# Kernel optimization log

Measured on AMD Instinct MI355X. Metric: run time of the kernel, lower is better.

The kernel has to match this reference:

```python
import jax, jax.numpy as jnp
import numpy as np

N = 100000       # nodes
E = 1600000      # edges (avg degree 16)
D_IN = 128
D_HID = 128      # 2 * out_channels
D_OUT = 64
BN_EPS = 1e-5
LRELU_SLOPE = 0.01
NORM_SCALE = 1.8


def setup_inputs() -> dict:
    key = jax.random.key(0)
    ks = jax.random.split(key, 8)
    x = jax.random.normal(ks[0], (N, D_IN), dtype=jnp.float32)
    edge_src = jax.random.randint(ks[1], (E,), 0, N)
    edge_dst = jax.random.randint(ks[2], (E,), 0, N)
    W1 = jax.random.normal(ks[3], (D_IN, D_HID), dtype=jnp.float32) / np.sqrt(D_IN).astype(np.float32)
    b1 = jnp.zeros((D_HID,), jnp.float32)
    gamma = jnp.ones((D_HID,), jnp.float32)
    beta = jnp.zeros((D_HID,), jnp.float32)
    Wmu = jax.random.normal(ks[4], (D_HID, D_OUT), dtype=jnp.float32) / np.sqrt(D_HID).astype(np.float32)
    bmu = jnp.zeros((D_OUT,), jnp.float32)
    noise = jax.random.normal(ks[5], (N, D_OUT), dtype=jnp.float32)
    return {"x": x, "edge_src": edge_src, "edge_dst": edge_dst, "W1": W1, "b1": b1,
            "gamma": gamma, "beta": beta, "Wmu": Wmu, "bmu": bmu, "noise": noise}


def appnp_k1(x, src, dst):
    """APPNP(K=1, alpha=0) == one symmetric GCN-normalized SpMM with self-loops."""
    ones = jnp.ones((src.shape[0],), x.dtype)
    deg = jax.ops.segment_sum(ones, dst, num_segments=N) + 1.0  # +1 for self-loop
    dinv = jax.lax.rsqrt(deg)
    w = dinv[src] * dinv[dst]                                   # [E] edge weights
    agg = jax.ops.segment_sum(x[src] * w[:, None], dst, num_segments=N)
    return agg + x * (dinv * dinv)[:, None]                     # self-loop term


def reference(x, edge_src, edge_dst, W1, b1, gamma, beta, Wmu, bmu, noise):
    # conv1 + propagate
    h = x @ W1 + b1                         # [N, D_HID]
    h = appnp_k1(h, edge_src, edge_dst)
    # BatchNorm1d (training mode: batch stats, biased variance)
    mean = h.mean(axis=0)
    var = h.var(axis=0)
    h = gamma * (h - mean) * jax.lax.rsqrt(var + BN_EPS) + beta
    # LeakyReLU
    h = jnp.where(h > 0, h, LRELU_SLOPE * h)
    # mu branch (convmu + propagate)
    l = h @ Wmu + bmu                       # [N, D_OUT]; used for both mu and logstd (original reuses convmu)
    mu = appnp_k1(l, edge_src, edge_dst)
    # logstd branch: F.normalize(convmu(h), p=2, dim=1) * 1.8 then propagate
    nrm = jnp.maximum(jnp.linalg.norm(l, axis=1, keepdims=True), 1e-12)
    logstd = appnp_k1(l / nrm * NORM_SCALE, edge_src, edge_dst)
    # reparam (training): mu + eps * exp(logstd)
    zeta = mu + noise * jnp.exp(logstd)
    return (mu, logstd, zeta)
```

## Files before the change

kernel.cpp:

```cpp
#include <hip/hip_runtime.h>
#include <hip/hip_bf16.h>
#include <math.h>

#define D_IN 128
#define D_HID 128
#define D_OUT 64
#define BN_EPS 1e-5f
#define SLOPE 0.01f
#define NSCALE 1.8f

#define BSH 8
#define NB 256
#define T1 4096
#define COLCAP 8192
#define LSTRIDE 192

typedef __attribute__((ext_vector_type(8))) short short8;
typedef __attribute__((ext_vector_type(4))) float f32x4;

__device__ inline void atomAddF(float* p, float v) {
#if defined(__gfx90a__) || defined(__gfx942__) || defined(__gfx950__)
    unsafeAtomicAdd(p, v);
#else
    atomicAdd(p, v);
#endif
}

__device__ inline ushort f2bf(float f) {
    union { float f; uint u; } v; v.f = f;
    uint r = v.u + 0x7fff + ((v.u >> 16) & 1);
    return (ushort)(r >> 16);
}
__device__ inline float bf2f(ushort b) {
    union { uint u; float f; } v; v.u = ((uint)b) << 16;
    return v.f;
}
__device__ inline float bflo(uint u) { return __uint_as_float(u << 16); }
__device__ inline float bfhi(uint u) { return __uint_as_float(u & 0xffff0000u); }

__device__ inline void add4(uint2 v, float a[4]) {
    a[0] += bflo(v.x); a[1] += bfhi(v.x);
    a[2] += bflo(v.y); a[3] += bfhi(v.y);
}
__device__ inline void fma4(uint2 v, float w, float a[4]) {
    a[0] = fmaf(bflo(v.x), w, a[0]);
    a[1] = fmaf(bfhi(v.x), w, a[1]);
    a[2] = fmaf(bflo(v.y), w, a[2]);
    a[3] = fmaf(bfhi(v.y), w, a[3]);
}
__device__ inline void acc8(uint4 v, float sv, float w, float am[8], float al[8]) {
    float e;
    e = bflo(v.x) * w; am[0] += e; al[0] = fmaf(e, sv, al[0]);
    e = bfhi(v.x) * w; am[1] += e; al[1] = fmaf(e, sv, al[1]);
    e = bflo(v.y) * w; am[2] += e; al[2] = fmaf(e, sv, al[2]);
    e = bfhi(v.y) * w; am[3] += e; al[3] = fmaf(e, sv, al[3]);
    e = bflo(v.z) * w; am[4] += e; al[4] = fmaf(e, sv, al[4]);
    e = bfhi(v.z) * w; am[5] += e; al[5] = fmaf(e, sv, al[5]);
    e = bflo(v.w) * w; am[6] += e; al[6] = fmaf(e, sv, al[6]);
    e = bfhi(v.w) * w; am[7] += e; al[7] = fmaf(e, sv, al[7]);
}

__global__ __launch_bounds__(256) void k_bhist(const int* __restrict__ dst,
        int* __restrict__ bcnt, int E, int B) {
    __shared__ int h[512];
    for (int i = threadIdx.x; i < 512; i += 256) h[i] = 0;
    __syncthreads();
    int beg = blockIdx.x * T1;
    int end = min(beg + T1, E);
    for (int e = beg + threadIdx.x; e < end; e += 256)
        atomicAdd(&h[dst[e] >> BSH], 1);
    __syncthreads();
    for (int i = threadIdx.x; i < B; i += 256)
        if (h[i]) atomicAdd(&bcnt[i], h[i]);
}

__global__ __launch_bounds__(512) void k_bscan(const int* __restrict__ bcnt,
        int* __restrict__ bbase, int* __restrict__ tailE, int B) {
    __shared__ int sh[512];
    int t = threadIdx.x;
    int v = (t < B) ? bcnt[t] : 0;
    sh[t] = v;
    __syncthreads();
    for (int o = 1; o < 512; o <<= 1) {
        int u = (t >= o) ? sh[t - o] : 0;
        __syncthreads();
        sh[t] += u;
        __syncthreads();
    }
    int excl = sh[t] - v;
    if (t < B) { bbase[t] = excl; tailE[t] = excl; }
    if (t == B - 1) bbase[B] = excl + v;
}

__global__ __launch_bounds__(256) void k_part(const int* __restrict__ src,
        const int* __restrict__ dst, int* __restrict__ tailE,
        uint* __restrict__ ep, int E, int B) {
    __shared__ int h[512], off[512], gb[512], cur[512];
    __shared__ int ps[256];
    __shared__ int2 ro[T1];
    int tid = threadIdx.x;
    for (int i = tid; i < 512; i += 256) h[i] = 0;
    __syncthreads();
    int beg = blockIdx.x * T1;
    int cnt = min(T1, E - beg);
    int s[16], d[16];
#pragma unroll
    for (int k = 0; k < 16; ++k) {
        int e = beg + tid + k * 256;
        if (e < E) {
            s[k] = src[e]; d[k] = dst[e];
            atomicAdd(&h[d[k] >> BSH], 1);
        } else d[k] = -1;
    }
    __syncthreads();
    int pa = h[2 * tid], pb = h[2 * tid + 1];
    ps[tid] = pa + pb;
    __syncthreads();
    int vv = ps[tid];
    for (int o = 1; o < 256; o <<= 1) {
        int u = (tid >= o) ? ps[tid - o] : 0;
        __syncthreads();
        ps[tid] += u;
        __syncthreads();
    }
    int excl = ps[tid] - vv;
    off[2 * tid] = excl;       off[2 * tid + 1] = excl + pa;
    cur[2 * tid] = excl;       cur[2 * tid + 1] = excl + pa;
    if (2 * tid < B && pa > 0)      gb[2 * tid] = atomicAdd(&tailE[2 * tid], pa);
    if (2 * tid + 1 < B && pb > 0)  gb[2 * tid + 1] = atomicAdd(&tailE[2 * tid + 1], pb);
    __syncthreads();
#pragma unroll
    for (int k = 0; k < 16; ++k) {
        if (d[k] >= 0) {
            int b = d[k] >> BSH;
            int p = atomicAdd(&cur[b], 1);
            ro[p] = make_int2(s[k], d[k]);
        }
    }
    __syncthreads();
    for (int i = tid; i < cnt; i += 256) {
        int2 e = ro[i];
        int b = e.y >> BSH;
        ep[gb[b] + (i - off[b])] = (uint)e.x | ((uint)(e.y & (NB - 1)) << 24);
    }
}

__global__ __launch_bounds__(256) void k_csr(const uint* __restrict__ ep,
        const int* __restrict__ bbase, int* __restrict__ rowptr,
        float* __restrict__ dinv, int* __restrict__ col, int n, int B) {
    int b = blockIdx.x;
    int lo = b << BSH;
    int hi = min(lo + NB, n);
    int nn = hi - lo;
    int ebeg = bbase[b], eend = bbase[b + 1], cnt = eend - ebeg;
    __shared__ int h[NB], pfx[NB], cur[NB];
    __shared__ int colbuf[COLCAP];
    int tid = threadIdx.x;
    if (tid < NB) h[tid] = 0;
    __syncthreads();
    for (int i = tid; i < cnt; i += 256)
        atomicAdd(&h[ep[ebeg + i] >> 24], 1);
    __syncthreads();
    int v = (tid < nn) ? h[tid] : 0;
    pfx[tid] = v;
    __syncthreads();
    for (int o = 1; o < 256; o <<= 1) {
        int u = (tid >= o) ? pfx[tid - o] : 0;
        __syncthreads();
        pfx[tid] += u;
        __syncthreads();
    }
    int excl = pfx[tid] - v;
    if (tid < nn) {
        rowptr[lo + tid] = ebeg + excl;
        dinv[lo + tid] = rsqrtf((float)v + 1.0f);
        cur[tid] = excl;
    }
    if (b == B - 1 && tid == 0) rowptr[n] = eend;
    __syncthreads();
    if (cnt <= COLCAP) {
        for (int i = tid; i < cnt; i += 256) {
            uint e = ep[ebeg + i];
            int p = atomicAdd(&cur[e >> 24], 1);
            colbuf[p] = (int)(e & 0xFFFFFFu);
        }
        __syncthreads();
        for (int i = tid; i < cnt; i += 256) col[ebeg + i] = colbuf[i];
    } else {
        for (int i = tid; i < cnt; i += 256) {
            uint e = ep[ebeg + i];
            int p = atomicAdd(&cur[e >> 24], 1);
            col[ebeg + p] = (int)(e & 0xFFFFFFu);
        }
    }
}

__global__ __launch_bounds__(256) void k_gemm1_mfma(const float* __restrict__ x,
        const float* __restrict__ W1, const float* __restrict__ b1,
        const float* __restrict__ dinv, ushort* __restrict__ h_bf, int n, int nwt) {
    __shared__ ushort wf[4][8][64][8];
    int t = threadIdx.x;
    for (int i = t; i < 16384; i += 256) {
        int k = i >> 7, nn = i & 127;
        int kt = k >> 5, ct = nn >> 4;
        int lane = ((k >> 3) & 3) * 16 + (nn & 15);
        int j = k & 7;
        wf[kt][ct][lane][j] = f2bf(W1[i]);
    }
    __syncthreads();
    size_t n64 = (size_t)n * 64;
    int wid = t >> 6, lane = t & 63;
    int lrow = lane & 15, lkg = lane >> 4;
    float bias[8];
#pragma unroll
    for (int ct = 0; ct < 8; ++ct) bias[ct] = b1[ct * 16 + lrow];
    int stride = gridDim.x * 4;
    for (int wt = blockIdx.x * 4 + wid; wt < nwt; wt += stride) {
        size_t r0 = (size_t)wt * 16;
        int rr = (int)r0 + lrow;
        if (rr >= n) rr = n - 1;
        short8 ah[4], al[4];
#pragma unroll
        for (int kt = 0; kt < 4; ++kt) {
            const float* p = x + (size_t)rr * 128 + kt * 32 + lkg * 8;
            float va[8];
            *(f32x4*)&va[0] = *(const f32x4*)p;
            *(f32x4*)&va[4] = *(const f32x4*)(p + 4);
#pragma unroll
            for (int j = 0; j < 8; ++j) {
                ushort hb = f2bf(va[j]);
                ah[kt][j] = (short)hb;
                al[kt][j] = (short)f2bf(va[j] - bf2f(hb));
            }
        }
        f32x4 acc[8];
#pragma unroll
        for (int ct = 0; ct < 8; ++ct) {
            float bb = bias[ct];
            acc[ct][0] = bb; acc[ct][1] = bb; acc[ct][2] = bb; acc[ct][3] = bb;
        }
#pragma unroll
        for (int kt = 0; kt < 4; ++kt) {
#pragma unroll
            for (int ct = 0; ct < 8; ++ct) {
                short8 wh = *(const short8*)&wf[kt][ct][lane][0];
                acc[ct] = __builtin_amdgcn_mfma_f32_16x16x32_bf16(ah[kt], wh, acc[ct], 0, 0, 0);
                acc[ct] = __builtin_amdgcn_mfma_f32_16x16x32_bf16(al[kt], wh, acc[ct], 0, 0, 0);
            }
        }
#pragma unroll
        for (int j = 0; j < 4; ++j) {
            int row = (int)r0 + lkg * 4 + j;
            if (row < n) {
                float dr = dinv[row];
#pragma unroll
                for (int ct = 0; ct < 8; ++ct)
                    h_bf[(size_t)(ct >> 2) * n64 + (size_t)row * 64 + (ct & 3) * 16 + lrow]
                        = f2bf(acc[ct][j] * dr);
            }
        }
    }
}

__global__ __launch_bounds__(512) void k_spmm1_csr(const int* __restrict__ rowptr,
        const int* __restrict__ col, const uint2* __restrict__ tbl,
        const float* __restrict__ dinv, uint2* __restrict__ aggq,
        float* __restrict__ accum, int n, int half) {
    __shared__ float red[8][16][4];
    int t = threadIdx.x;
    int wid = t >> 6, lane = t & 63;
    int q = lane >> 4, g = lane & 15;
    int gw = blockIdx.x * 8 + wid;
    int nw = gridDim.x * 8;
    float sx[4] = {0.f, 0.f, 0.f, 0.f}, sq[4] = {0.f, 0.f, 0.f, 0.f};
    for (int node = gw; node < n; node += nw) {
        int beg = rowptr[node], end = rowptr[node + 1];
        float a[4] = {0.f, 0.f, 0.f, 0.f};
        if (q == 0) add4(tbl[(size_t)node * 16 + g], a);
        int p = beg;
        for (; p + 16 <= end; p += 16) {
            int c0 = col[p + q], c1 = col[p + 4 + q];
            int c2 = col[p + 8 + q], c3 = col[p + 12 + q];
            uint2 v0 = tbl[(size_t)c0 * 16 + g];
            uint2 v1 = tbl[(size_t)c1 * 16 + g];
            uint2 v2 = tbl[(size_t)c2 * 16 + g];
            uint2 v3 = tbl[(size_t)c3 * 16 + g];
            add4(v0, a); add4(v1, a); add4(v2, a); add4(v3, a);
        }
        if (p + 8 <= end) {
            int c0 = col[p + q], c1 = col[p + 4 + q];
            uint2 v0 = tbl[(size_t)c0 * 16 + g];
            uint2 v1 = tbl[(size_t)c1 * 16 + g];
            add4(v0, a); add4(v1, a);
            p += 8;
        }
        if (p < end) {
            int i0 = p + q, i1 = p + 4 + q;
            int c0 = col[i0 < end ? i0 : end - 1];
            int c1 = col[i1 < end ? i1 : end - 1];
            float w0 = (i0 < end) ? 1.f : 0.f;
            float w1 = (i1 < end) ? 1.f : 0.f;
            fma4(tbl[(size_t)c0 * 16 + g], w0, a);
            fma4(tbl[(size_t)c1 * 16 + g], w1, a);
        }
#pragma unroll
        for (int j = 0; j < 4; ++j) {
            a[j] += __shfl_xor(a[j], 16, 64);
            a[j] += __shfl_xor(a[j], 32, 64);
        }
        if (q == 0) {
            float di = dinv[node];
#pragma unroll
            for (int j = 0; j < 4; ++j) a[j] *= di;
            uint2 pk;
            pk.x = ((uint)f2bf(a[1]) << 16) | (uint)f2bf(a[0]);
            pk.y = ((uint)f2bf(a[3]) << 16) | (uint)f2bf(a[2]);
            aggq[(size_t)node * 32 + half * 16 + g] = pk;
#pragma unroll
            for (int j = 0; j < 4; ++j) {
                sx[j] += a[j];
                sq[j] = fmaf(a[j], a[j], sq[j]);
            }
        }
    }
    if (q == 0) {
#pragma unroll
        for (int j = 0; j < 4; ++j) red[wid][g][j] = sx[j];
    }
    __syncthreads();
    if (t < 64) {
        float v = 0.f;
        for (int w = 0; w < 8; ++w) v += red[w][t >> 2][t & 3];
        atomAddF(&accum[half * 64 + t], v);
    }
    __syncthreads();
    if (q == 0) {
#pragma unroll
        for (int j = 0; j < 4; ++j) red[wid][g][j] = sq[j];
    }
    __syncthreads();
    if (t < 64) {
        float v = 0.f;
        for (int w = 0; w < 8; ++w) v += red[w][t >> 2][t & 3];
        atomAddF(&accum[128 + half * 64 + t], v);
    }
}

__global__ __launch_bounds__(256) void k_gemm2_mfma(const ushort* __restrict__ agg_bf,
        const float* __restrict__ Wmu, const float* __restrict__ bmu,
        const float* __restrict__ accum, const float* __restrict__ gamma,
        const float* __restrict__ beta, const float* __restrict__ dinv,
        char* __restrict__ l_ext, float inv_n, int n, int nwt) {
    __shared__ ushort wf[4][4][64][8];
    __shared__ float scs[D_HID], shs[D_HID];
    int t = threadIdx.x;
    for (int i = t; i < 8192; i += 256) {
        int k = i >> 6, nn = i & 63;
        int kt = k >> 5, ct = nn >> 4;
        int lane = ((k >> 3) & 3) * 16 + (nn & 15);
        int j = k & 7;
        wf[kt][ct][lane][j] = f2bf(Wmu[i]);
    }
    for (int i = t; i < D_HID; i += 256) {
        float mean = accum[i] * inv_n;
        float var = accum[D_HID + i] * inv_n - mean * mean;
        float sc = gamma[i] * rsqrtf(var + BN_EPS);
        scs[i] = sc;
        shs[i] = beta[i] - mean * sc;
    }
    __syncthreads();
    int wid = t >> 6, lane = t & 63;
    int lrow = lane & 15, lkg = lane >> 4;
    float bias[4];
#pragma unroll
    for (int ct = 0; ct < 4; ++ct) bias[ct] = bmu[ct * 16 + lrow];
    int stride = gridDim.x * 4;
    for (int wt = blockIdx.x * 4 + wid; wt < nwt; wt += stride) {
        size_t r0 = (size_t)wt * 16;
        int rr = (int)r0 + lrow;
        if (rr >= n) rr = n - 1;
        short8 ah[4], al[4];
#pragma unroll
        for (int kt = 0; kt < 4; ++kt) {
            const ushort* p = agg_bf + (size_t)rr * 128 + kt * 32 + lkg * 8;
            short8 raw = *(const short8*)p;
#pragma unroll
            for (int j = 0; j < 8; ++j) {
                int k = kt * 32 + lkg * 8 + j;
                float v = bf2f((ushort)raw[j]) * scs[k] + shs[k];
                v = v > 0.f ? v : SLOPE * v;
                ushort hb = f2bf(v);
                ah[kt][j] = (short)hb;
                al[kt][j] = (short)f2bf(v - bf2f(hb));
            }
        }
        f32x4 acc[4];
#pragma unroll
        for (int ct = 0; ct < 4; ++ct) {
            float bb = bias[ct];
            acc[ct][0] = bb; acc[ct][1] = bb; acc[ct][2] = bb; acc[ct][3] = bb;
        }
#pragma unroll
        for (int kt = 0; kt < 4; ++kt) {
#pragma unroll
            for (int ct = 0; ct < 4; ++ct) {
                short8 wh = *(const short8*)&wf[kt][ct][lane][0];
                acc[ct] = __builtin_amdgcn_mfma_f32_16x16x32_bf16(ah[kt], wh, acc[ct], 0, 0, 0);
                acc[ct] = __builtin_amdgcn_mfma_f32_16x16x32_bf16(al[kt], wh, acc[ct], 0, 0, 0);
            }
        }
#pragma unroll
        for (int j = 0; j < 4; ++j) {
            float ss = acc[0][j] * acc[0][j];
#pragma unroll
            for (int ct = 1; ct < 4; ++ct) ss = fmaf(acc[ct][j], acc[ct][j], ss);
            ss += __shfl_xor(ss, 1, 64);
            ss += __shfl_xor(ss, 2, 64);
            ss += __shfl_xor(ss, 4, 64);
            ss += __shfl_xor(ss, 8, 64);
            float srow = NSCALE / fmaxf(sqrtf(ss), 1e-12f);
            int row = (int)r0 + lkg * 4 + j;
            if (row < n) {
                float dr = dinv[row];
                char* base = l_ext + (size_t)row * LSTRIDE;
#pragma unroll
                for (int ct = 0; ct < 4; ++ct)
                    *(ushort*)(base + (ct * 16 + lrow) * 2) = f2bf(acc[ct][j] * dr);
                if (lrow == 0) *(float*)(base + 128) = srow;
            }
        }
    }
}

__global__ __launch_bounds__(512) void k_spmm2_csr(const int* __restrict__ rowptr,
        const int* __restrict__ col, const char* __restrict__ lb,
        const float* __restrict__ dinv, const float* __restrict__ noise,
        float* __restrict__ mu, float* __restrict__ lsd, float* __restrict__ zeta,
        int n) {
    int node = blockIdx.x * 8 + ((int)threadIdx.x >> 6);
    if (node >= n) return;
    int lane = threadIdx.x & 63;
    int oct = lane >> 3, g = lane & 7;
    int beg = rowptr[node], end = rowptr[node + 1];
    float am[8], al[8];
#pragma unroll
    for (int j = 0; j < 8; ++j) { am[j] = 0.f; al[j] = 0.f; }
    if (oct == 0) {
        const char* rb = lb + (size_t)node * LSTRIDE;
        uint4 v = *(const uint4*)(rb + g * 16);
        float sv = *(const float*)(rb + 128);
        acc8(v, sv, 1.f, am, al);
    }
    int p = beg;
    for (; p + 16 <= end; p += 16) {
        int c0 = col[p + oct], c1 = col[p + 8 + oct];
        const char* r0 = lb + (size_t)c0 * LSTRIDE;
        const char* r1 = lb + (size_t)c1 * LSTRIDE;
        uint4 v0 = *(const uint4*)(r0 + g * 16);
        float s0 = *(const float*)(r0 + 128);
        uint4 v1 = *(const uint4*)(r1 + g * 16);
        float s1 = *(const float*)(r1 + 128);
        acc8(v0, s0, 1.f, am, al);
        acc8(v1, s1, 1.f, am, al);
    }
    if (p + 8 <= end) {
        int c0 = col[p + oct];
        const char* r0 = lb + (size_t)c0 * LSTRIDE;
        uint4 v0 = *(const uint4*)(r0 + g * 16);
        float s0 = *(const float*)(r0 + 128);
        acc8(v0, s0, 1.f, am, al);
        p += 8;
    }
    if (p < end) {
        int i0 = p + oct;
        int c0 = col[i0 < end ? i0 : end - 1];
        float w0 = (i0 < end) ? 1.f : 0.f;
        const char* r0 = lb + (size_t)c0 * LSTRIDE;
        uint4 v0 = *(const uint4*)(r0 + g * 16);
        float s0 = *(const float*)(r0 + 128);
        acc8(v0, s0, w0, am, al);
    }
#pragma unroll
    for (int j = 0; j < 8; ++j) {
        am[j] += __shfl_xor(am[j], 8, 64);
        am[j] += __shfl_xor(am[j], 16, 64);
        am[j] += __shfl_xor(am[j], 32, 64);
        al[j] += __shfl_xor(al[j], 8, 64);
        al[j] += __shfl_xor(al[j], 16, 64);
        al[j] += __shfl_xor(al[j], 32, 64);
    }
    if (lane < 8) {
        float di = dinv[node];
        size_t idx = (size_t)node * 64 + lane * 8;
        f32x4 m0, m1, l0, l1, z0, z1;
#pragma unroll
        for (int j = 0; j < 4; ++j) {
            m0[j] = am[j] * di;     m1[j] = am[j + 4] * di;
            l0[j] = al[j] * di;     l1[j] = al[j + 4] * di;
        }
        f32x4 n0 = *(const f32x4*)(noise + idx);
        f32x4 n1 = *(const f32x4*)(noise + idx + 4);
#pragma unroll
        for (int j = 0; j < 4; ++j) {
            z0[j] = m0[j] + n0[j] * expf(l0[j]);
            z1[j] = m1[j] + n1[j] * expf(l1[j]);
        }
        *(f32x4*)(mu + idx) = m0;   *(f32x4*)(mu + idx + 4) = m1;
        *(f32x4*)(lsd + idx) = l0;  *(f32x4*)(lsd + idx + 4) = l1;
        *(f32x4*)(zeta + idx) = z0; *(f32x4*)(zeta + idx + 4) = z1;
    }
}

extern "C" void kernel_launch(void* const* d_in, const int* in_sizes, int n_in,
                              void* d_out, int out_size, void* d_ws, size_t ws_size,
                              hipStream_t stream) {
    const float* x     = (const float*)d_in[0];
    const int*   esrc  = (const int*)d_in[1];
    const int*   edst  = (const int*)d_in[2];
    const float* W1    = (const float*)d_in[3];
    const float* b1    = (const float*)d_in[4];
    const float* gamma = (const float*)d_in[5];
    const float* beta  = (const float*)d_in[6];
    const float* Wmu   = (const float*)d_in[7];
    const float* bmu   = (const float*)d_in[8];
    const float* noise = (const float*)d_in[9];
    int N = in_sizes[0] / D_IN;
    int E = in_sizes[1];
    int B = (N + NB - 1) >> BSH;
    int nwt = (N + 15) / 16;
    int ntile = (E + T1 - 1) / T1;

    float* out  = (float*)d_out;
    float* mu   = out;
    float* lsd  = out + (size_t)N * D_OUT;
    float* zeta = out + 2 * (size_t)N * D_OUT;

    char* ws = (char*)d_ws;
    size_t off = 0;
    auto alloc = [&](size_t bytes) {
        void* p = ws + off;
        off += (bytes + 255) & ~(size_t)255;
        return p;
    };
    float* accum  = (float*)alloc(1024);
    int* bcnt     = (int*)alloc((size_t)B * 4);
    size_t zbytes = off;
    int* bbase    = (int*)alloc(((size_t)B + 1) * 4);
    int* tailE    = (int*)alloc((size_t)B * 4);
    int* rowptr   = (int*)alloc(((size_t)N + 1) * 4);
    float* dinv   = (float*)alloc((size_t)N * 4);
    uint* ep      = (uint*)alloc((size_t)E * 4);
    int* col      = (int*)alloc((size_t)E * 4);
    ushort* h_bf  = (ushort*)alloc((size_t)N * D_HID * 2);
    uint2* aggq   = (uint2*)alloc((size_t)N * D_HID * 2);
    char* l_ext   = (char*)alloc((size_t)N * LSTRIDE);

    hipMemsetAsync(d_ws, 0, zbytes, stream);

    size_t n64 = (size_t)N * 64;
    const uint2* tbl0 = (const uint2*)h_bf;
    const uint2* tbl1 = (const uint2*)(h_bf + n64);

    k_bhist<<<ntile, 256, 0, stream>>>(edst, bcnt, E, B);
    k_bscan<<<1, 512, 0, stream>>>(bcnt, bbase, tailE, B);
    k_part<<<ntile, 256, 0, stream>>>(esrc, edst, tailE, ep, E, B);
    k_csr<<<B, 256, 0, stream>>>(ep, bbase, rowptr, dinv, col, N, B);
    k_gemm1_mfma<<<512, 256, 0, stream>>>(x, W1, b1, dinv, h_bf, N, nwt);
    k_spmm1_csr<<<2048, 512, 0, stream>>>(rowptr, col, tbl0, dinv, aggq, accum, N, 0);
    k_spmm1_csr<<<2048, 512, 0, stream>>>(rowptr, col, tbl1, dinv, aggq, accum, N, 1);
    k_gemm2_mfma<<<512, 256, 0, stream>>>((const ushort*)aggq, Wmu, bmu, accum,
                                          gamma, beta, dinv, l_ext, 1.0f / (float)N, N, nwt);
    k_spmm2_csr<<<(N + 7) / 8, 512, 0, stream>>>(rowptr, col, l_ext, dinv, noise, mu, lsd, zeta, N);
}
```

Baseline: 311.6 us.

## Map one 16-lane group per node in both SpMM kernels, dropping cross-lane reductions

Both SpMM kernels now assign a 16-thread group to each destination node, with every lane walking all of that node's edges serially, instead of splitting edges across the 4 or 8 lane groups of a wavefront and combining them with shuffles. This removes the shuffle reductions and leaves no lanes idle during the epilogue, and it lets each kernel handle four times as many nodes per block. In exchange, each lane issues more dependent gather loads per node, and the memory access per node is narrower (uint2 rather than uint4 in spmm2). The BatchNorm statistics reduction now uses shared-memory atomics instead of a per-wave array.

New measurement: 355.4 us. 1.14x slower.

```diff
diff --git a/kernel.cpp b/kernel.cpp
--- a/kernel.cpp
+++ b/kernel.cpp
@@ -48,16 +48,12 @@
     a[2] = fmaf(bflo(v.y), w, a[2]);
     a[3] = fmaf(bfhi(v.y), w, a[3]);
 }
-__device__ inline void acc8(uint4 v, float sv, float w, float am[8], float al[8]) {
+__device__ inline void dacc4(uint2 v, float sv, float w, float am[4], float al[4]) {
     float e;
     e = bflo(v.x) * w; am[0] += e; al[0] = fmaf(e, sv, al[0]);
     e = bfhi(v.x) * w; am[1] += e; al[1] = fmaf(e, sv, al[1]);
     e = bflo(v.y) * w; am[2] += e; al[2] = fmaf(e, sv, al[2]);
     e = bfhi(v.y) * w; am[3] += e; al[3] = fmaf(e, sv, al[3]);
-    e = bflo(v.z) * w; am[4] += e; al[4] = fmaf(e, sv, al[4]);
-    e = bfhi(v.z) * w; am[5] += e; al[5] = fmaf(e, sv, al[5]);
-    e = bflo(v.w) * w; am[6] += e; al[6] = fmaf(e, sv, al[6]);
-    e = bfhi(v.w) * w; am[7] += e; al[7] = fmaf(e, sv, al[7]);
 }
 
 __global__ __launch_bounds__(256) void k_bhist(const int* __restrict__ dst,
@@ -266,83 +262,65 @@
         const int* __restrict__ col, const uint2* __restrict__ tbl,
         const float* __restrict__ dinv, uint2* __restrict__ aggq,
         float* __restrict__ accum, int n, int half) {
-    __shared__ float red[8][16][4];
+    __shared__ float redx[64], redq[64];
     int t = threadIdx.x;
-    int wid = t >> 6, lane = t & 63;
-    int q = lane >> 4, g = lane & 15;
-    int gw = blockIdx.x * 8 + wid;
-    int nw = gridDim.x * 8;
+    if (t < 64) { redx[t] = 0.f; redq[t] = 0.f; }
+    __syncthreads();
+    int grp = t >> 4, lid = t & 15;
+    int nstride = gridDim.x * 32;
     float sx[4] = {0.f, 0.f, 0.f, 0.f}, sq[4] = {0.f, 0.f, 0.f, 0.f};
-    for (int node = gw; node < n; node += nw) {
+    for (int node = blockIdx.x * 32 + grp; node < n; node += nstride) {
         int beg = rowptr[node], end = rowptr[node + 1];
         float a[4] = {0.f, 0.f, 0.f, 0.f};
-        if (q == 0) add4(tbl[(size_t)node * 16 + g], a);
+        add4(tbl[(size_t)node * 16 + lid], a);
         int p = beg;
-        for (; p + 16 <= end; p += 16) {
-            int c0 = col[p + q], c1 = col[p + 4 + q];
-            int c2 = col[p + 8 + q], c3 = col[p + 12 + q];
-            uint2 v0 = tbl[(size_t)c0 * 16 + g];
-            uint2 v1 = tbl[(size_t)c1 * 16 + g];
-            uint2 v2 = tbl[(size_t)c2 * 16 + g];
-            uint2 v3 = tbl[(size_t)c3 * 16 + g];
+        for (; p + 8 <= end; p += 8) {
+            int c0 = col[p],     c1 = col[p + 1], c2 = col[p + 2], c3 = col[p + 3];
+            int c4 = col[p + 4], c5 = col[p + 5], c6 = col[p + 6], c7 = col[p + 7];
+            uint2 v0 = tbl[(size_t)c0 * 16 + lid];
+            uint2 v1 = tbl[(size_t)c1 * 16 + lid];
+            uint2 v2 = tbl[(size_t)c2 * 16 + lid];
+            uint2 v3 = tbl[(size_t)c3 * 16 + lid];
+            uint2 v4 = tbl[(size_t)c4 * 16 + lid];
+            uint2 v5 = tbl[(size_t)c5 * 16 + lid];
+            uint2 v6 = tbl[(size_t)c6 * 16 + lid];
+            uint2 v7 = tbl[(size_t)c7 * 16 + lid];
             add4(v0, a); add4(v1, a); add4(v2, a); add4(v3, a);
-        }
-        if (p + 8 <= end) {
-            int c0 = col[p + q], c1 = col[p + 4 + q];
-            uint2 v0 = tbl[(size_t)c0 * 16 + g];
-            uint2 v1 = tbl[(size_t)c1 * 16 + g];
-            add4(v0, a); add4(v1, a);
-            p += 8;
-        }
-        if (p < end) {
-            int i0 = p + q, i1 = p + 4 + q;
-            int c0 = col[i0 < end ? i0 : end - 1];
-            int c1 = col[i1 < end ? i1 : end - 1];
-            float w0 = (i0 < end) ? 1.f : 0.f;
-            float w1 = (i1 < end) ? 1.f : 0.f;
-            fma4(tbl[(size_t)c0 * 16 + g], w0, a);
-            fma4(tbl[(size_t)c1 * 16 + g], w1, a);
-        }
+            add4(v4, a); add4(v5, a); add4(v6, a); add4(v7, a);
+        }
+        if (p + 4 <= end) {
+            int c0 = col[p], c1 = col[p + 1], c2 = col[p + 2], c3 = col[p + 3];
+            uint2 v0 = tbl[(size_t)c0 * 16 + lid];
+            uint2 v1 = tbl[(size_t)c1 * 16 + lid];
+            uint2 v2 = tbl[(size_t)c2 * 16 + lid];
+            uint2 v3 = tbl[(size_t)c3 * 16 + lid];
+            add4(v0, a); add4(v1, a); add4(v2, a); add4(v3, a);
+            p += 4;
+        }
+        for (; p < end; ++p)
+            add4(tbl[(size_t)col[p] * 16 + lid], a);
+        float di = dinv[node];
+#pragma unroll
+        for (int j = 0; j < 4; ++j) a[j] *= di;
+        uint2 pk;
+        pk.x = ((uint)f2bf(a[1]) << 16) | (uint)f2bf(a[0]);
+        pk.y = ((uint)f2bf(a[3]) << 16) | (uint)f2bf(a[2]);
+        aggq[(size_t)node * 32 + half * 16 + lid] = pk;
 #pragma unroll
         for (int j = 0; j < 4; ++j) {
-            a[j] += __shfl_xor(a[j], 16, 64);
-            a[j] += __shfl_xor(a[j], 32, 64);
-        }
-        if (q == 0) {
-            float di = dinv[node];
-#pragma unroll
-            for (int j = 0; j < 4; ++j) a[j] *= di;
-            uint2 pk;
-            pk.x = ((uint)f2bf(a[1]) << 16) | (uint)f2bf(a[0]);
-            pk.y = ((uint)f2bf(a[3]) << 16) | (uint)f2bf(a[2]);
-            aggq[(size_t)node * 32 + half * 16 + g] = pk;
-#pragma unroll
-            for (int j = 0; j < 4; ++j) {
-                sx[j] += a[j];
-                sq[j] = fmaf(a[j], a[j], sq[j]);
-            }
-        }
-    }
-    if (q == 0) {
-#pragma unroll
-        for (int j = 0; j < 4; ++j) red[wid][g][j] = sx[j];
+            sx[j] += a[j];
+            sq[j] = fmaf(a[j], a[j], sq[j]);
+        }
+    }
+#pragma unroll
+    for (int j = 0; j < 4; ++j) {
+        atomicAdd(&redx[lid * 4 + j], sx[j]);
+        atomicAdd(&redq[lid * 4 + j], sq[j]);
     }
     __syncthreads();
     if (t < 64) {
-        float v = 0.f;
-        for (int w = 0; w < 8; ++w) v += red[w][t >> 2][t & 3];
-        atomAddF(&accum[half * 64 + t], v);
-    }
-    __syncthreads();
-    if (q == 0) {
-#pragma unroll
-        for (int j = 0; j < 4; ++j) red[wid][g][j] = sq[j];
-    }
-    __syncthreads();
-    if (t < 64) {
-        float v = 0.f;
-        for (int w = 0; w < 8; ++w) v += red[w][t >> 2][t & 3];
-        atomAddF(&accum[128 + half * 64 + t], v);
+        atomAddF(&accum[half * 64 + t], redx[t]);
+        atomAddF(&accum[128 + half * 64 + t], redq[t]);
     }
 }
 
@@ -437,78 +415,74 @@
         const float* __restrict__ dinv, const float* __restrict__ noise,
         float* __restrict__ mu, float* __restrict__ lsd, float* __restrict__ zeta,
         int n) {
-    int node = blockIdx.x * 8 + ((int)threadIdx.x >> 6);
+    int t = threadIdx.x;
+    int grp = t >> 4, lid = t & 15;
+    int node = blockIdx.x * 32 + grp;
     if (node >= n) return;
-    int lane = threadIdx.x & 63;
-    int oct = lane >> 3, g = lane & 7;
     int beg = rowptr[node], end = rowptr[node + 1];
-    float am[8], al[8];
-#pragma unroll
-    for (int j = 0; j < 8; ++j) { am[j] = 0.f; al[j] = 0.f; }
-    if (oct == 0) {
+    float am[4] = {0.f, 0.f, 0.f, 0.f}, al[4] = {0.f, 0.f, 0.f, 0.f};
+    {
         const char* rb = lb + (size_t)node * LSTRIDE;
-        uint4 v = *(const uint4*)(rb + g * 16);
+        uint2 v = *(const uint2*)(rb + lid * 8);
         float sv = *(const float*)(rb + 128);
-        acc8(v, sv, 1.f, am, al);
+        dacc4(v, sv, 1.f, am, al);
     }
     int p = beg;
-    for (; p + 16 <= end; p += 16) {
-        int c0 = col[p + oct], c1 = col[p + 8 + oct];
+    for (; p + 8 <= end; p += 8) {
+        int c0 = col[p],     c1 = col[p + 1], c2 = col[p + 2], c3 = col[p + 3];
+        int c4 = col[p + 4], c5 = col[p + 5], c6 = col[p + 6], c7 = col[p + 7];
         const char* r0 = lb + (size_t)c0 * LSTRIDE;
         const char* r1 = lb + (size_t)c1 * LSTRIDE;
-        uint4 v0 = *(const uint4*)(r0 + g * 16);
+        const char* r2 = lb + (size_t)c2 * LSTRIDE;
+        const char* r3 = lb + (size_t)c3 * LSTRIDE;
+        const char* r4 = lb + (size_t)c4 * LSTRIDE;
+        const char* r5 = lb + (size_t)c5 * LSTRIDE;
+        const char* r6 = lb + (size_t)c6 * LSTRIDE;
+        const char* r7 = lb + (size_t)c7 * LSTRIDE;
+        uint2 v0 = *(const uint2*)(r0 + lid * 8); float s0 = *(const float*)(r0 + 128);
+        uint2 v1 = *(const uint2*)(r1 + lid * 8); float s1 = *(const float*)(r1 + 128);
+        uint2 v2 = *(const uint2*)(r2 + lid * 8); float s2 = *(const float*)(r2 + 128);
+        uint2 v3 = *(const uint2*)(r3 + lid * 8); float s3 = *(const float*)(r3 + 128);
+        uint2 v4 = *(const uint2*)(r4 + lid * 8); float s4 = *(const float*)(r4 + 128);
+        uint2 v5 = *(const uint2*)(r5 + lid * 8); float s5 = *(const float*)(r5 + 128);
+        uint2 v6 = *(const uint2*)(r6 + lid * 8); float s6 = *(const float*)(r6 + 128);
+        uint2 v7 = *(const uint2*)(r7 + lid * 8); float s7 = *(const float*)(r7 + 128);
+        dacc4(v0, s0, 1.f, am, al); dacc4(v1, s1, 1.f, am, al);
+        dacc4(v2, s2, 1.f, am, al); dacc4(v3, s3, 1.f, am, al);
+        dacc4(v4, s4, 1.f, am, al); dacc4(v5, s5, 1.f, am, al);
+        dacc4(v6, s6, 1.f, am, al); dacc4(v7, s7, 1.f, am, al);
+    }
+    if (p + 4 <= end) {
+        int c0 = col[p], c1 = col[p + 1], c2 = col[p + 2], c3 = col[p + 3];
+        const char* r0 = lb + (size_t)c0 * LSTRIDE;
+        const char* r1 = lb + (size_t)c1 * LSTRIDE;
+        const char* r2 = lb + (size_t)c2 * LSTRIDE;
+        const char* r3 = lb + (size_t)c3 * LSTRIDE;
+        uint2 v0 = *(const uint2*)(r0 + lid * 8); float s0 = *(const float*)(r0 + 128);
+        uint2 v1 = *(const uint2*)(r1 + lid * 8); float s1 = *(const float*)(r1 + 128);
+        uint2 v2 = *(const uint2*)(r2 + lid * 8); float s2 = *(const float*)(r2 + 128);
+        uint2 v3 = *(const uint2*)(r3 + lid * 8); float s3 = *(const float*)(r3 + 128);
+        dacc4(v0, s0, 1.f, am, al); dacc4(v1, s1, 1.f, am, al);
+        dacc4(v2, s2, 1.f, am, al); dacc4(v3, s3, 1.f, am, al);
+        p += 4;
+    }
+    for (; p < end; ++p) {
+        const char* r0 = lb + (size_t)col[p] * LSTRIDE;
+        uint2 v0 = *(const uint2*)(r0 + lid * 8);
         float s0 = *(const float*)(r0 + 128);
-        uint4 v1 = *(const uint4*)(r1 + g * 16);
-        float s1 = *(const float*)(r1 + 128);
-        acc8(v0, s0, 1.f, am, al);
-        acc8(v1, s1, 1.f, am, al);
-    }
-    if (p + 8 <= end) {
-        int c0 = col[p + oct];
-        const char* r0 = lb + (size_t)c0 * LSTRIDE;
-        uint4 v0 = *(const uint4*)(r0 + g * 16);
-        float s0 = *(const float*)(r0 + 128);
-        acc8(v0, s0, 1.f, am, al);
-        p += 8;
-    }
-    if (p < end) {
-        int i0 = p + oct;
-        int c0 = col[i0 < end ? i0 : end - 1];
-        float w0 = (i0 < end) ? 1.f : 0.f;
-        const char* r0 = lb + (size_t)c0 * LSTRIDE;
-        uint4 v0 = *(const uint4*)(r0 + g * 16);
-        float s0 = *(const float*)(r0 + 128);
-        acc8(v0, s0, w0, am, al);
-    }
-#pragma unroll
-    for (int j = 0; j < 8; ++j) {
-        am[j] += __shfl_xor(am[j], 8, 64);
-        am[j] += __shfl_xor(am[j], 16, 64);
-        am[j] += __shfl_xor(am[j], 32, 64);
-        al[j] += __shfl_xor(al[j], 8, 64);
-        al[j] += __shfl_xor(al[j], 16, 64);
-        al[j] += __shfl_xor(al[j], 32, 64);
-    }
-    if (lane < 8) {
-        float di = dinv[node];
-        size_t idx = (size_t)node * 64 + lane * 8;
-        f32x4 m0, m1, l0, l1, z0, z1;
-#pragma unroll
-        for (int j = 0; j < 4; ++j) {
-            m0[j] = am[j] * di;     m1[j] = am[j + 4] * di;
-            l0[j] = al[j] * di;     l1[j] = al[j + 4] * di;
-        }
-        f32x4 n0 = *(const f32x4*)(noise + idx);
-        f32x4 n1 = *(const f32x4*)(noise + idx + 4);
-#pragma unroll
-        for (int j = 0; j < 4; ++j) {
-            z0[j] = m0[j] + n0[j] * expf(l0[j]);
-            z1[j] = m1[j] + n1[j] * expf(l1[j]);
-        }
-        *(f32x4*)(mu + idx) = m0;   *(f32x4*)(mu + idx + 4) = m1;
-        *(f32x4*)(lsd + idx) = l0;  *(f32x4*)(lsd + idx + 4) = l1;
-        *(f32x4*)(zeta + idx) = z0; *(f32x4*)(zeta + idx + 4) = z1;
-    }
+        dacc4(v0, s0, 1.f, am, al);
+    }
+    float di = dinv[node];
+    size_t idx = (size_t)node * 64 + lid * 4;
+    f32x4 m, l, z;
+#pragma unroll
+    for (int j = 0; j < 4; ++j) { m[j] = am[j] * di; l[j] = al[j] * di; }
+    f32x4 nz = *(const f32x4*)(noise + idx);
+#pragma unroll
+    for (int j = 0; j < 4; ++j) z[j] = m[j] + nz[j] * expf(l[j]);
+    *(f32x4*)(mu + idx) = m;
+    *(f32x4*)(lsd + idx) = l;
+    *(f32x4*)(zeta + idx) = z;
 }
 
 extern "C" void kernel_launch(void* const* d_in, const int* in_sizes, int n_in,
@@ -570,5 +544,5 @@
     k_spmm1_csr<<<2048, 512, 0, stream>>>(rowptr, col, tbl1, dinv, aggq, accum, N, 1);
     k_gemm2_mfma<<<512, 256, 0, stream>>>((const ushort*)aggq, Wmu, bmu, accum,
                                           gamma, beta, dinv, l_ext, 1.0f / (float)N, N, nwt);
-    k_spmm2_csr<<<(N + 7) / 8, 512, 0, stream>>>(rowptr, col, l_ext, dinv, noise, mu, lsd, zeta, N);
-}
+    k_spmm2_csr<<<(N + 31) / 32, 512, 0, stream>>>(rowptr, col, l_ext, dinv, noise, mu, lsd, zeta, N);
+}
```

## Switch SpMM gathers to fp16 packed math and merge halved SpMM1 passes

Applied to the files above, without the earlier changes.

Intermediate feature tables are now stored as fp16 instead of bf16. The gathers accumulate with packed half2 add and fma instead of unpacking to fp32, and the cross-lane reductions in SpMM2 run on half2 as well. The two half-width SpMM1 launches are merged into one pass over the full 128-wide row using 16-byte loads, which halves the CSR/index traffic and the launch count. The cost is reduced accumulation precision: fp16 sums over about 17 neighbours carry a risk of overflow or tolerance failures.

Measured after the change: 271.5 us. 1.15x faster.

```diff
diff --git a/kernel.cpp b/kernel.cpp
--- a/kernel.cpp
+++ b/kernel.cpp
@@ -1,5 +1,6 @@
 #include <hip/hip_runtime.h>
 #include <hip/hip_bf16.h>
+#include <hip/hip_fp16.h>
 #include <math.h>
 
 #define D_IN 128
@@ -35,29 +36,29 @@
     union { uint u; float f; } v; v.u = ((uint)b) << 16;
     return v.f;
 }
-__device__ inline float bflo(uint u) { return __uint_as_float(u << 16); }
-__device__ inline float bfhi(uint u) { return __uint_as_float(u & 0xffff0000u); }
-
-__device__ inline void add4(uint2 v, float a[4]) {
-    a[0] += bflo(v.x); a[1] += bfhi(v.x);
-    a[2] += bflo(v.y); a[3] += bfhi(v.y);
-}
-__device__ inline void fma4(uint2 v, float w, float a[4]) {
-    a[0] = fmaf(bflo(v.x), w, a[0]);
-    a[1] = fmaf(bfhi(v.x), w, a[1]);
-    a[2] = fmaf(bflo(v.y), w, a[2]);
-    a[3] = fmaf(bfhi(v.y), w, a[3]);
-}
-__device__ inline void acc8(uint4 v, float sv, float w, float am[8], float al[8]) {
-    float e;
-    e = bflo(v.x) * w; am[0] += e; al[0] = fmaf(e, sv, al[0]);
-    e = bfhi(v.x) * w; am[1] += e; al[1] = fmaf(e, sv, al[1]);
-    e = bflo(v.y) * w; am[2] += e; al[2] = fmaf(e, sv, al[2]);
-    e = bfhi(v.y) * w; am[3] += e; al[3] = fmaf(e, sv, al[3]);
-    e = bflo(v.z) * w; am[4] += e; al[4] = fmaf(e, sv, al[4]);
-    e = bfhi(v.z) * w; am[5] += e; al[5] = fmaf(e, sv, al[5]);
-    e = bflo(v.w) * w; am[6] += e; al[6] = fmaf(e, sv, al[6]);
-    e = bfhi(v.w) * w; am[7] += e; al[7] = fmaf(e, sv, al[7]);
+__device__ inline ushort f2h(float f) {
+    __half h = __float2half_rn(f);
+    return *reinterpret_cast<ushort*>(&h);
+}
+__device__ inline __half2 u2h2(uint u) { return *reinterpret_cast<__half2*>(&u); }
+__device__ inline __half2 shfl_xor_h2(__half2 v, int m) {
+    int iv = *reinterpret_cast<int*>(&v);
+    int r = __shfl_xor(iv, m, 64);
+    return *reinterpret_cast<__half2*>(&r);
+}
+
+__device__ inline void phadd8(uint4 v, __half2 a[4]) {
+    a[0] = __hadd2(a[0], u2h2(v.x));
+    a[1] = __hadd2(a[1], u2h2(v.y));
+    a[2] = __hadd2(a[2], u2h2(v.z));
+    a[3] = __hadd2(a[3], u2h2(v.w));
+}
+__device__ inline void pdacc8(uint4 v, __half2 s2, __half2 am[4], __half2 al[4]) {
+    __half2 h0 = u2h2(v.x), h1 = u2h2(v.y), h2 = u2h2(v.z), h3 = u2h2(v.w);
+    am[0] = __hadd2(am[0], h0); al[0] = __hfma2(h0, s2, al[0]);
+    am[1] = __hadd2(am[1], h1); al[1] = __hfma2(h1, s2, al[1]);
+    am[2] = __hadd2(am[2], h2); al[2] = __hfma2(h2, s2, al[2]);
+    am[3] = __hadd2(am[3], h3); al[3] = __hfma2(h3, s2, al[3]);
 }
 
 __global__ __launch_bounds__(256) void k_bhist(const int* __restrict__ dst,
@@ -197,7 +198,7 @@
 
 __global__ __launch_bounds__(256) void k_gemm1_mfma(const float* __restrict__ x,
         const float* __restrict__ W1, const float* __restrict__ b1,
-        const float* __restrict__ dinv, ushort* __restrict__ h_bf, int n, int nwt) {
+        const float* __restrict__ dinv, ushort* __restrict__ h16, int n, int nwt) {
     __shared__ ushort wf[4][8][64][8];
     int t = threadIdx.x;
     for (int i = t; i < 16384; i += 256) {
@@ -208,7 +209,6 @@
         wf[kt][ct][lane][j] = f2bf(W1[i]);
     }
     __syncthreads();
-    size_t n64 = (size_t)n * 64;
     int wid = t >> 6, lane = t & 63;
     int lrow = lane & 15, lkg = lane >> 4;
     float bias[8];
@@ -255,69 +255,79 @@
                 float dr = dinv[row];
 #pragma unroll
                 for (int ct = 0; ct < 8; ++ct)
-                    h_bf[(size_t)(ct >> 2) * n64 + (size_t)row * 64 + (ct & 3) * 16 + lrow]
-                        = f2bf(acc[ct][j] * dr);
+                    h16[(size_t)row * 128 + ct * 16 + lrow] = f2h(acc[ct][j] * dr);
             }
         }
     }
 }
 
 __global__ __launch_bounds__(512) void k_spmm1_csr(const int* __restrict__ rowptr,
-        const int* __restrict__ col, const uint2* __restrict__ tbl,
-        const float* __restrict__ dinv, uint2* __restrict__ aggq,
-        float* __restrict__ accum, int n, int half) {
-    __shared__ float red[8][16][4];
+        const int* __restrict__ col, const uint4* __restrict__ tbl,
+        const float* __restrict__ dinv, uint4* __restrict__ agg4,
+        float* __restrict__ accum, int n) {
+    __shared__ float red[8][16][8];
     int t = threadIdx.x;
     int wid = t >> 6, lane = t & 63;
     int q = lane >> 4, g = lane & 15;
     int gw = blockIdx.x * 8 + wid;
     int nw = gridDim.x * 8;
-    float sx[4] = {0.f, 0.f, 0.f, 0.f}, sq[4] = {0.f, 0.f, 0.f, 0.f};
+    float sx[8], sq[8];
+#pragma unroll
+    for (int j = 0; j < 8; ++j) { sx[j] = 0.f; sq[j] = 0.f; }
+    __half2 hz = __float2half2_rn(0.f);
     for (int node = gw; node < n; node += nw) {
         int beg = rowptr[node], end = rowptr[node + 1];
-        float a[4] = {0.f, 0.f, 0.f, 0.f};
-        if (q == 0) add4(tbl[(size_t)node * 16 + g], a);
+        __half2 a2[4] = {hz, hz, hz, hz};
+        if (q == 0) phadd8(tbl[(size_t)node * 16 + g], a2);
         int p = beg;
         for (; p + 16 <= end; p += 16) {
             int c0 = col[p + q], c1 = col[p + 4 + q];
             int c2 = col[p + 8 + q], c3 = col[p + 12 + q];
-            uint2 v0 = tbl[(size_t)c0 * 16 + g];
-            uint2 v1 = tbl[(size_t)c1 * 16 + g];
-            uint2 v2 = tbl[(size_t)c2 * 16 + g];
-            uint2 v3 = tbl[(size_t)c3 * 16 + g];
-            add4(v0, a); add4(v1, a); add4(v2, a); add4(v3, a);
+            uint4 v0 = tbl[(size_t)c0 * 16 + g];
+            uint4 v1 = tbl[(size_t)c1 * 16 + g];
+            uint4 v2 = tbl[(size_t)c2 * 16 + g];
+            uint4 v3 = tbl[(size_t)c3 * 16 + g];
+            phadd8(v0, a2); phadd8(v1, a2); phadd8(v2, a2); phadd8(v3, a2);
         }
         if (p + 8 <= end) {
             int c0 = col[p + q], c1 = col[p + 4 + q];
-            uint2 v0 = tbl[(size_t)c0 * 16 + g];
-            uint2 v1 = tbl[(size_t)c1 * 16 + g];
-            add4(v0, a); add4(v1, a);
+            uint4 v0 = tbl[(size_t)c0 * 16 + g];
+            uint4 v1 = tbl[(size_t)c1 * 16 + g];
+            phadd8(v0, a2); phadd8(v1, a2);
             p += 8;
         }
         if (p < end) {
             int i0 = p + q, i1 = p + 4 + q;
             int c0 = col[i0 < end ? i0 : end - 1];
             int c1 = col[i1 < end ? i1 : end - 1];
-            float w0 = (i0 < end) ? 1.f : 0.f;
-            float w1 = (i1 < end) ? 1.f : 0.f;
-            fma4(tbl[(size_t)c0 * 16 + g], w0, a);
-            fma4(tbl[(size_t)c1 * 16 + g], w1, a);
-        }
+            uint4 v0 = tbl[(size_t)c0 * 16 + g];
+            uint4 v1 = tbl[(size_t)c1 * 16 + g];
+            if (i0 < end) phadd8(v0, a2);
+            if (i1 < end) phadd8(v1, a2);
+        }
+        float a[8];
 #pragma unroll
         for (int j = 0; j < 4; ++j) {
+            float2 f = __half22float2(a2[j]);
+            a[2 * j] = f.x; a[2 * j + 1] = f.y;
+        }
+#pragma unroll
+        for (int j = 0; j < 8; ++j) {
             a[j] += __shfl_xor(a[j], 16, 64);
             a[j] += __shfl_xor(a[j], 32, 64);
         }
         if (q == 0) {
             float di = dinv[node];
 #pragma unroll
-            for (int j = 0; j < 4; ++j) a[j] *= di;
-            uint2 pk;
+            for (int j = 0; j < 8; ++j) a[j] *= di;
+            uint4 pk;
             pk.x = ((uint)f2bf(a[1]) << 16) | (uint)f2bf(a[0]);
             pk.y = ((uint)f2bf(a[3]) << 16) | (uint)f2bf(a[2]);
-            aggq[(size_t)node * 32 + half * 16 + g] = pk;
-#pragma unroll
-            for (int j = 0; j < 4; ++j) {
+            pk.z = ((uint)f2bf(a[5]) << 16) | (uint)f2bf(a[4]);
+            pk.w = ((uint)f2bf(a[7]) << 16) | (uint)f2bf(a[6]);
+            agg4[(size_t)node * 16 + g] = pk;
+#pragma unroll
+            for (int j = 0; j < 8; ++j) {
                 sx[j] += a[j];
                 sq[j] = fmaf(a[j], a[j], sq[j]);
             }
@@ -325,24 +335,24 @@
     }
     if (q == 0) {
 #pragma unroll
-        for (int j = 0; j < 4; ++j) red[wid][g][j] = sx[j];
-    }
-    __syncthreads();
-    if (t < 64) {
+        for (int j = 0; j < 8; ++j) red[wid][g][j] = sx[j];
+    }
+    __syncthreads();
+    if (t < 128) {
         float v = 0.f;
-        for (int w = 0; w < 8; ++w) v += red[w][t >> 2][t & 3];
-        atomAddF(&accum[half * 64 + t], v);
+        for (int w = 0; w < 8; ++w) v += red[w][t >> 3][t & 7];
+        atomAddF(&accum[t], v);
     }
     __syncthreads();
     if (q == 0) {
 #pragma unroll
-        for (int j = 0; j < 4; ++j) red[wid][g][j] = sq[j];
-    }
-    __syncthreads();
-    if (t < 64) {
+        for (int j = 0; j < 8; ++j) red[wid][g][j] = sq[j];
+    }
+    __syncthreads();
+    if (t < 128) {
         float v = 0.f;
-        for (int w = 0; w < 8; ++w) v += red[w][t >> 2][t & 3];
-        atomAddF(&accum[128 + half * 64 + t], v);
+        for (int w = 0; w < 8; ++w) v += red[w][t >> 3][t & 7];
+        atomAddF(&accum[128 + t], v);
     }
 }
 
@@ -425,8 +435,8 @@
                 char* base = l_ext + (size_t)row * LSTRIDE;
 #pragma unroll
                 for (int ct = 0; ct < 4; ++ct)
-                    *(ushort*)(base + (ct * 16 + lrow) * 2) = f2bf(acc[ct][j] * dr);
-                if (lrow == 0) *(float*)(base + 128) = srow;
+                    *(ushort*)(base + (ct * 16 + lrow) * 2) = f2h(acc[ct][j] * dr);
+                if (lrow == 0) *(ushort*)(base + 128) = f2h(srow);
             }
         }
     }
@@ -442,14 +452,14 @@
     int lane = threadIdx.x & 63;
     int oct = lane >> 3, g = lane & 7;
     int beg = rowptr[node], end = rowptr[node + 1];
-    float am[8], al[8];
-#pragma unroll
-    for (int j = 0; j < 8; ++j) { am[j] = 0.f; al[j] = 0.f; }
+    __half2 hz = __float2half2_rn(0.f);
+    __half2 am2[4] = {hz, hz, hz, hz}, al2[4] = {hz, hz, hz, hz};
     if (oct == 0) {
         const char* rb = lb + (size_t)node * LSTRIDE;
         uint4 v = *(const uint4*)(rb + g * 16);
-        float sv = *(const float*)(rb + 128);
-        acc8(v, sv, 1.f, am, al);
+        ushort sr = *(const ushort*)(rb + 128);
+        __half2 s2 = __half2half2(*reinterpret_cast<const __half*>(&sr));
+        pdacc8(v, s2, am2, al2);
     }
     int p = beg;
     for (; p + 16 <= end; p += 16) {
@@ -457,51 +467,59 @@
         const char* r0 = lb + (size_t)c0 * LSTRIDE;
         const char* r1 = lb + (size_t)c1 * LSTRIDE;
         uint4 v0 = *(const uint4*)(r0 + g * 16);
-        float s0 = *(const float*)(r0 + 128);
+        ushort sr0 = *(const ushort*)(r0 + 128);
         uint4 v1 = *(const uint4*)(r1 + g * 16);
-        float s1 = *(const float*)(r1 + 128);
-        acc8(v0, s0, 1.f, am, al);
-        acc8(v1, s1, 1.f, am, al);
+        ushort sr1 = *(const ushort*)(r1 + 128);
+        __half2 s20 = __half2half2(*reinterpret_cast<const __half*>(&sr0));
+        __half2 s21 = __half2half2(*reinterpret_cast<const __half*>(&sr1));
+        pdacc8(v0, s20, am2, al2);
+        pdacc8(v1, s21, am2, al2);
     }
     if (p + 8 <= end) {
         int c0 = col[p + oct];
         const char* r0 = lb + (size_t)c0 * LSTRIDE;
         uint4 v0 = *(const uint4*)(r0 + g * 16);
-        float s0 = *(const float*)(r0 + 128);
-        acc8(v0, s0, 1.f, am, al);
+        ushort sr0 = *(const ushort*)(r0 + 128);
+        __half2 s20 = __half2half2(*reinterpret_cast<const __half*>(&sr0));
+        pdacc8(v0, s20, am2, al2);
         p += 8;
     }
     if (p < end) {
         int i0 = p + oct;
         int c0 = col[i0 < end ? i0 : end - 1];
-        float w0 = (i0 < end) ? 1.f : 0.f;
         const char* r0 = lb + (size_t)c0 * LSTRIDE;
         uint4 v0 = *(const uint4*)(r0 + g * 16);
-        float s0 = *(const float*)(r0 + 128);
-        acc8(v0, s0, w0, am, al);
-    }
-#pragma unroll
-    for (int j = 0; j < 8; ++j) {
-        am[j] += __shfl_xor(am[j], 8, 64);
-        am[j] += __shfl_xor(am[j], 16, 64);
-        am[j] += __shfl_xor(am[j], 32, 64);
-        al[j] += __shfl_xor(al[j], 8, 64);
-        al[j] += __shfl_xor(al[j], 16, 64);
-        al[j] += __shfl_xor(al[j], 32, 64);
+        ushort sr0 = *(const ushort*)(r0 + 128);
+        __half2 s20 = __half2half2(*reinterpret_cast<const __half*>(&sr0));
+        if (i0 < end) pdacc8(v0, s20, am2, al2);
+    }
+#pragma unroll
+    for (int j = 0; j < 4; ++j) {
+        am2[j] = __hadd2(am2[j], shfl_xor_h2(am2[j], 8));
+        am2[j] = __hadd2(am2[j], shfl_xor_h2(am2[j], 16));
+        am2[j] = __hadd2(am2[j], shfl_xor_h2(am2[j], 32));
+        al2[j] = __hadd2(al2[j], shfl_xor_h2(al2[j], 8));
+        al2[j] = __hadd2(al2[j], shfl_xor_h2(al2[j], 16));
+        al2[j] = __hadd2(al2[j], shfl_xor_h2(al2[j], 32));
     }
     if (lane < 8) {
         float di = dinv[node];
         size_t idx = (size_t)node * 64 + lane * 8;
-        f32x4 m0, m1, l0, l1, z0, z1;
+        float am[8], al[8];
 #pragma unroll
         for (int j = 0; j < 4; ++j) {
-            m0[j] = am[j] * di;     m1[j] = am[j + 4] * di;
-            l0[j] = al[j] * di;     l1[j] = al[j + 4] * di;
+            float2 fm = __half22float2(am2[j]);
+            float2 fl = __half22float2(al2[j]);
+            am[2 * j] = fm.x * di; am[2 * j + 1] = fm.y * di;
+            al[2 * j] = fl.x * di; al[2 * j + 1] = fl.y * di;
         }
         f32x4 n0 = *(const f32x4*)(noise + idx);
         f32x4 n1 = *(const f32x4*)(noise + idx + 4);
+        f32x4 m0, m1, l0, l1, z0, z1;
 #pragma unroll
         for (int j = 0; j < 4; ++j) {
+            m0[j] = am[j];     m1[j] = am[j + 4];
+            l0[j] = al[j];     l1[j] = al[j + 4];
             z0[j] = m0[j] + n0[j] * expf(l0[j]);
             z1[j] = m1[j] + n1[j] * expf(l1[j]);
         }
@@ -551,24 +569,19 @@
     float* dinv   = (float*)alloc((size_t)N * 4);
     uint* ep      = (uint*)alloc((size_t)E * 4);
     int* col      = (int*)alloc((size_t)E * 4);
-    ushort* h_bf  = (ushort*)alloc((size_t)N * D_HID * 2);
-    uint2* aggq   = (uint2*)alloc((size_t)N * D_HID * 2);
+    ushort* h16   = (ushort*)alloc((size_t)N * D_HID * 2);
+    uint4* agg4   = (uint4*)alloc((size_t)N * D_HID * 2);
     char* l_ext   = (char*)alloc((size_t)N * LSTRIDE);
 
     hipMemsetAsync(d_ws, 0, zbytes, stream);
-
-    size_t n64 = (size_t)N * 64;
-    const uint2* tbl0 = (const uint2*)h_bf;
-    const uint2* tbl1 = (const uint2*)(h_bf + n64);
 
     k_bhist<<<ntile, 256, 0, stream>>>(edst, bcnt, E, B);
     k_bscan<<<1, 512, 0, stream>>>(bcnt, bbase, tailE, B);
     k_part<<<ntile, 256, 0, stream>>>(esrc, edst, tailE, ep, E, B);
     k_csr<<<B, 256, 0, stream>>>(ep, bbase, rowptr, dinv, col, N, B);
-    k_gemm1_mfma<<<512, 256, 0, stream>>>(x, W1, b1, dinv, h_bf, N, nwt);
-    k_spmm1_csr<<<2048, 512, 0, stream>>>(rowptr, col, tbl0, dinv, aggq, accum, N, 0);
-    k_spmm1_csr<<<2048, 512, 0, stream>>>(rowptr, col, tbl1, dinv, aggq, accum, N, 1);
-    k_gemm2_mfma<<<512, 256, 0, stream>>>((const ushort*)aggq, Wmu, bmu, accum,
+    k_gemm1_mfma<<<512, 256, 0, stream>>>(x, W1, b1, dinv, h16, N, nwt);
+    k_spmm1_csr<<<2048, 512, 0, stream>>>(rowptr, col, (const uint4*)h16, dinv, agg4, accum, N);
+    k_gemm2_mfma<<<512, 256, 0, stream>>>((const ushort*)agg4, Wmu, bmu, accum,
                                           gamma, beta, dinv, l_ext, 1.0f / (float)N, N, nwt);
     k_spmm2_csr<<<(N + 7) / 8, 512, 0, stream>>>(rowptr, col, l_ext, dinv, noise, mu, lsd, zeta, N);
 }
```
